# Performance work log

Hardware: AMD Instinct MI355X
Metric: run time of the kernel (lower is better)

## Reference

```python
import jax, jax.numpy as jnp
import numpy as np

LOGISTIC_R = 3.8
COUPLING_ITERS = 5


def _linear_interp(v, L):
    """PyTorch F.interpolate(mode='linear', align_corners=False) along last axis.
    v: [..., K] real -> [..., L] real."""
    K = v.shape[-1]
    pos = (jnp.arange(L, dtype=jnp.float32) + 0.5) * (K / L) - 0.5
    pos = jnp.clip(pos, 0.0, K - 1)  # torch clamps src coords into range
    i0 = jnp.floor(pos).astype(jnp.int32)
    i1 = jnp.minimum(i0 + 1, K - 1)
    w = pos - i0
    return v[..., i0] * (1.0 - w) + v[..., i1] * w


def setup_inputs() -> dict:
    key = jax.random.key(0)
    ks = jax.random.split(key, 4)
    B, Cin, Cout, L, K = 16, 64, 64, 8192, 64
    return {
        "x_real": jax.random.normal(ks[0], (B, Cin, L), jnp.float32),
        "x_imag": jax.random.normal(ks[1], (B, Cin, L), jnp.float32),
        "kernel_real": jax.random.normal(ks[2], (Cout, Cin, K), jnp.float32),
        "kernel_imag": jax.random.normal(ks[3], (Cout, Cin, K), jnp.float32),
        "alpha_D": jnp.ones((1,), jnp.float32),
    }


def reference(x_real, x_imag, kernel_real, kernel_imag, alpha_D):
    x = x_real + 1j * x_imag  # [B, Cin, L] complex64
    L = x.shape[-1]

    # --- logistic self-coupling on magnitude (per-batch min/max over (C, L)) ---
    mag = jnp.abs(x)
    phase = jnp.angle(x)
    mmin = mag.min(axis=(-1, -2), keepdims=True)
    mmax = mag.max(axis=(-1, -2), keepdims=True)
    xn = (mag - mmin) / (mmax - mmin + 1e-10)
    for _ in range(COUPLING_ITERS):
        xn = LOGISTIC_R * xn * (1.0 - xn)
    mag_c = xn * (mmax - mmin) + mmin
    x_coupled = mag_c * jnp.exp(1j * phase)

    # --- spectral conv: FFT, per-pair kernel interpolation, complex MAC ---
    x_fft = jnp.fft.fft(x_coupled, axis=-1)  # [B, Cin, L]
    kfft = jnp.fft.fft(kernel_real + 1j * kernel_imag, axis=-1)  # [O, I, K]
    kmag = _linear_interp(jnp.abs(kfft), L)    # [O, I, L]
    kph = _linear_interp(jnp.angle(kfft), L)   # [O, I, L]
    kint = kmag * jnp.exp(1j * kph)            # [O, I, L] complex64
    out_fft = jnp.einsum('bjl,ijl->bil', x_fft, kint)  # replaces O*I python loop
    out = jnp.fft.ifft(out_fft, axis=-1)  # [B, O, L]

    # --- optical probe activation: sin(omega*0 + phi0 + alpha_D * lambda) ---
    theta = alpha_D[0] * jnp.arange(L, dtype=jnp.float32)
    act = jnp.sin(theta)  # omega*t = 0, phi0 = 0
    return out * act
```

## Files before the change

### kernel.cpp

```cpp
#include <hip/hip_runtime.h>
#include <hip/hip_fp16.h>
#include <hip/hip_bf16.h>
#include <math.h>

#define L 8192
#define LOG2L 13
#define B 16
#define CIN 64
#define COUT 64
#define KK 64

#define PI_F 3.14159265358979323846f

typedef float f4v __attribute__((ext_vector_type(4)));
typedef short s8v __attribute__((ext_vector_type(8)));

__device__ __forceinline__ int PHI(int n) { return n ^ ((((n >> 5) ^ (n >> 9)) & 15) << 1); }

__device__ __forceinline__ void nsincos(float ang, float* sn, float* cs) {
    float r = ang * 0.15915494309189535f;
    r = r - floorf(r);
    *sn = __builtin_amdgcn_sinf(r);
    *cs = __builtin_amdgcn_cosf(r);
}

__device__ __forceinline__ unsigned short f2bf(float f) {
    unsigned u = __builtin_bit_cast(unsigned, f);
    u += 0x7FFFu + ((u >> 16) & 1u);
    return (unsigned short)(u >> 16);
}
__device__ __forceinline__ unsigned pkbf(float a, float b) {
    unsigned ua = __builtin_bit_cast(unsigned, a) + 0x8000u;
    unsigned ub = __builtin_bit_cast(unsigned, b) + 0x8000u;
    return (ub & 0xFFFF0000u) | (ua >> 16);
}
__device__ __forceinline__ float bf_lo(unsigned u) {
    return __builtin_bit_cast(float, u << 16);
}
__device__ __forceinline__ float bf_hi(unsigned u) {
    return __builtin_bit_cast(float, u & 0xFFFF0000u);
}

template<int INV>
__device__ __forceinline__ void bfly4(float& u0r, float& u0i, float& u1r, float& u1i,
                                      float& v0r, float& v0i, float& v1r, float& v1i,
                                      float w1r, float w1i, float w2r, float w2i) {
    float A0r = u0r + v0r, A0i = u0i + v0i;
    float t0r = u0r - v0r, t0i = u0i - v0i;
    float B0r = t0r * w1r - t0i * w1i, B0i = t0r * w1i + t0i * w1r;
    float A1r = u1r + v1r, A1i = u1i + v1i;
    float t1r = u1r - v1r, t1i = u1i - v1i;
    float wr = t1r * w1r - t1i * w1i, wi = t1r * w1i + t1i * w1r;
    float B1r = INV ? -wi : wi;
    float B1i = INV ? wr : -wr;
    u0r = A0r + A1r; u0i = A0i + A1i;
    float d0r = A0r - A1r, d0i = A0i - A1i;
    u1r = d0r * w2r - d0i * w2i; u1i = d0r * w2i + d0i * w2r;
    v0r = B0r + B1r; v0i = B0i + B1i;
    float d1r = B0r - B1r, d1i = B0i - B1i;
    v1r = d1r * w2r - d1i * w2i; v1i = d1r * w2i + d1i * w2r;
}

template<int INV>
__device__ __forceinline__ void radix16(float* xr, float* xi, float wc, float ws) {
    const float C8 = 0.9238795325112867f, S8 = 0.3826834323650898f, C4 = 0.7071067811865476f;
    float e1r = C8, e1i = INV ? S8 : -S8;
    float e2r = C4, e2i = INV ? C4 : -C4;
    float e3r = S8, e3i = INV ? C8 : -C8;
    float a1r[4], a1i[4], a2r[4], a2i[4];
    a1r[0] = wc;                    a1i[0] = ws;
    a1r[1] = wc * e1r - ws * e1i;   a1i[1] = wc * e1i + ws * e1r;
    a1r[2] = wc * e2r - ws * e2i;   a1i[2] = wc * e2i + ws * e2r;
    a1r[3] = wc * e3r - ws * e3i;   a1i[3] = wc * e3i + ws * e3r;
#pragma unroll
    for (int q = 0; q < 4; ++q) {
        a2r[q] = a1r[q] * a1r[q] - a1i[q] * a1i[q];
        a2i[q] = 2.f * a1r[q] * a1i[q];
    }
    float b1r = a2r[0] * a2r[0] - a2i[0] * a2i[0], b1i = 2.f * a2r[0] * a2i[0];
    float b2r = b1r * b1r - b1i * b1i, b2i = 2.f * b1r * b1i;
#pragma unroll
    for (int q = 0; q < 4; ++q)
        bfly4<INV>(xr[q], xi[q], xr[q + 4], xi[q + 4], xr[q + 8], xi[q + 8],
                   xr[q + 12], xi[q + 12], a1r[q], a1i[q], a2r[q], a2i[q]);
#pragma unroll
    for (int c = 0; c < 4; ++c)
        bfly4<INV>(xr[4 * c], xi[4 * c], xr[4 * c + 1], xi[4 * c + 1],
                   xr[4 * c + 2], xi[4 * c + 2], xr[4 * c + 3], xi[4 * c + 3],
                   b1r, b1i, b2r, b2i);
}

__global__ __launch_bounds__(256) void k_reduce1(const float* __restrict__ xr,
                                                 const float* __restrict__ xi,
                                                 float* __restrict__ pmin,
                                                 float* __restrict__ pmax) {
    int bid = blockIdx.x;
    int batch = bid >> 6, slice = bid & 63;
    size_t base = (size_t)batch * CIN * L + (size_t)slice * L;
    int tid = threadIdx.x;
    float mn = 3.4e38f, mx = 0.0f;
    for (int r = 0; r < 32; ++r) {
        int idx = r * 256 + tid;
        float a = xr[base + idx], b = xi[base + idx];
        float m = sqrtf(a * a + b * b);
        mn = fminf(mn, m);
        mx = fmaxf(mx, m);
    }
    __shared__ float smn[4], smx[4];
    for (int off = 32; off >= 1; off >>= 1) {
        mn = fminf(mn, __shfl_down(mn, off));
        mx = fmaxf(mx, __shfl_down(mx, off));
    }
    int wave = tid >> 6;
    if ((tid & 63) == 0) { smn[wave] = mn; smx[wave] = mx; }
    __syncthreads();
    if (tid == 0) {
        for (int w = 1; w < 4; ++w) { mn = fminf(mn, smn[w]); mx = fmaxf(mx, smx[w]); }
        pmin[bid] = mn;
        pmax[bid] = mx;
    }
}

__global__ __launch_bounds__(64) void k_reduce2(const float* __restrict__ pmin,
                                                const float* __restrict__ pmax,
                                                float* __restrict__ mmin,
                                                float* __restrict__ mmax) {
    int b = blockIdx.x, t = threadIdx.x;
    float mn = pmin[b * 64 + t], mx = pmax[b * 64 + t];
    for (int off = 32; off >= 1; off >>= 1) {
        mn = fminf(mn, __shfl_down(mn, off));
        mx = fmaxf(mx, __shfl_down(mx, off));
    }
    if (t == 0) { mmin[b] = mn; mmax[b] = mx; }
}

__global__ __launch_bounds__(64) void k_kstats(const float* __restrict__ kr,
                                               const float* __restrict__ ki,
                                               float* __restrict__ Pmag,
                                               float* __restrict__ Pph) {
    int row = blockIdx.x;
    int k = threadIdx.x;
    __shared__ float sr[64], si[64];
    sr[k] = kr[row * 64 + k];
    si[k] = ki[row * 64 + k];
    __syncthreads();
    float ar = 0.f, ai = 0.f;
    for (int n = 0; n < 64; ++n) {
        int m = (n * k) & 63;
        float ang = -2.0f * PI_F * (float)m * (1.0f / 64.0f);
        float s, c;
        __sincosf(ang, &s, &c);
        ar += sr[n] * c - si[n] * s;
        ai += sr[n] * s + si[n] * c;
    }
    float mag = sqrtf(ar * ar + ai * ai);
    float ph = atan2f(ai, ar);
    int io = row >> 6, jn = row & 63;
    int ic = io >> 4, l15 = io & 15;
    int jc = jn >> 5, hi = (jn >> 3) & 3, e = jn & 7;
    int lane = hi * 16 + l15;
    size_t off = (size_t)k * 4096 + (ic * 2 + jc) * 512 + lane * 8 + e;
    Pmag[off] = mag;
    Pph[off] = ph;
    if (k == 63) {
        Pmag[off + 4096] = mag;
        Pph[off + 4096] = ph;
    }
}

__global__ __launch_bounds__(512) void k_fwd(const float* __restrict__ xr,
                                             const float* __restrict__ xi,
                                             const float* __restrict__ mmin_,
                                             const float* __restrict__ mmax_,
                                             unsigned* __restrict__ Xd) {
    __shared__ unsigned sPk[L];
    int row = blockIdx.x;
    int b = row >> 6;
    int tid = threadIdx.x;
    float mmin = mmin_[b], mmax = mmax_[b];
    float span = mmax - mmin;
    float invden = 1.0f / (span + 1e-10f);
    size_t base = (size_t)row * L;

    float vr[16], vi[16];
#pragma unroll
    for (int r = 0; r < 16; ++r) {
        int idx = r * 512 + tid;
        float a = xr[base + idx], c = xi[base + idx];
        float m2 = a * a + c * c;
        float rinv = (m2 > 0.0f) ? __builtin_amdgcn_rsqf(m2) : 0.0f;
        float m = m2 * rinv;
        float xn = (m - mmin) * invden;
#pragma unroll
        for (int it = 0; it < 5; ++it) xn = 3.8f * xn * (1.0f - xn);
        float mc = xn * span + mmin;
        float scale = mc * rinv;
        vr[r] = a * scale;
        vi[r] = c * scale;
    }
    {
        const float ER = 0.9238795325112867f, EI = -0.3826834323650898f;
        float wr_, wi_;
        nsincos(-PI_F * (float)tid * (1.0f / 4096.0f), &wi_, &wr_);
#pragma unroll
        for (int r = 0; r < 8; ++r) {
            float ar = vr[r], ai = vi[r], br = vr[r + 8], bi = vi[r + 8];
            vr[r] = ar + br; vi[r] = ai + bi;
            float dr = ar - br, di = ai - bi;
            vr[r + 8] = dr * wr_ - di * wi_;
            vi[r + 8] = dr * wi_ + di * wr_;
            float nr = wr_ * ER - wi_ * EI;
            wi_ = wr_ * EI + wi_ * ER;
            wr_ = nr;
        }
    }
#pragma unroll
    for (int r = 0; r < 16; ++r)
        sPk[PHI(r * 512 + tid)] = pkbf(vr[r], vi[r]);
    __syncthreads();

    {
        int j1 = tid & 255, bA = (tid >> 8) << 12;
#pragma unroll
        for (int m = 0; m < 16; ++m) {
            unsigned u = sPk[PHI(bA + j1 + (m << 8))];
            vr[m] = bf_lo(u); vi[m] = bf_hi(u);
        }
        float sn, cs;
        nsincos(-PI_F * (float)j1 * (1.0f / 2048.0f), &sn, &cs);
        radix16<0>(vr, vi, cs, sn);
#pragma unroll
        for (int m = 0; m < 16; ++m)
            sPk[PHI(bA + j1 + (m << 8))] = pkbf(vr[m], vi[m]);
    }
    __syncthreads();
    {
        int j1 = tid & 15, bB = (tid >> 4) << 8;
#pragma unroll
        for (int m = 0; m < 16; ++m) {
            unsigned u = sPk[PHI(bB + j1 + (m << 4))];
            vr[m] = bf_lo(u); vi[m] = bf_hi(u);
        }
        float sn, cs;
        nsincos(-PI_F * (float)j1 * (1.0f / 128.0f), &sn, &cs);
        radix16<0>(vr, vi, cs, sn);
#pragma unroll
        for (int m = 0; m < 16; ++m)
            sPk[PHI(bB + j1 + (m << 4))] = pkbf(vr[m], vi[m]);
    }
    __syncthreads();
    {
        uint2* s2 = (uint2*)sPk;
#pragma unroll
        for (int m = 0; m < 8; ++m) {
            int a = PHI(tid * 16 + 2 * m) >> 1;
            uint2 u2 = s2[a];
            vr[2 * m] = bf_lo(u2.x); vi[2 * m] = bf_hi(u2.x);
            vr[2 * m + 1] = bf_lo(u2.y); vi[2 * m + 1] = bf_hi(u2.y);
        }
        radix16<0>(vr, vi, 1.0f, 0.0f);
#pragma unroll
        for (int m = 0; m < 8; ++m) {
            int a = PHI(tid * 16 + 2 * m) >> 1;
            s2[a] = make_uint2(pkbf(vr[2 * m], vi[2 * m]),
                               pkbf(vr[2 * m + 1], vi[2 * m + 1]));
        }
    }
    __syncthreads();

    {
        int rt = (int)(__brev((unsigned)tid) >> 23);
        unsigned o16[16];
#pragma unroll
        for (int r = 0; r < 16; ++r) {
            int pi = (int)(__brev((unsigned)r) >> 28);
            o16[pi] = sPk[PHI(r * 512 + rt)];
        }
        size_t ob = (size_t)tid * 16384 + (size_t)row * 16;
#pragma unroll
        for (int k = 0; k < 4; ++k)
            *(uint4*)&Xd[ob + 4 * k] = make_uint4(o16[4 * k], o16[4 * k + 1],
                                                  o16[4 * k + 2], o16[4 * k + 3]);
    }
}

#define PBG 8
#define REG 4624
__global__ __launch_bounds__(256) void k_gemm(const unsigned* __restrict__ X,
                                              const float* __restrict__ Pmag,
                                              const float* __restrict__ Pph,
                                              unsigned* __restrict__ outd) {
    __shared__ uint4 ldsbuf[(PBG * REG) / 16];
    char* lds = (char*)ldsbuf;
    int tid = threadIdx.x;
    int bid = blockIdx.x;
    int pwin = ((bid & 7) << 7) + (bid >> 3);
    int p0 = pwin * PBG;
    int half = pwin & 1;
    const unsigned* src = X + (size_t)(pwin >> 1) * 16384 + half * 8;

#pragma unroll
    for (int k = 0; k < 8; ++k) {
        int u = k * 256 + tid;
        int row = u >> 1;
        int g = u & 1;
        uint4 v = *(const uint4*)&src[(size_t)row * 16 + g * 4];
        int base = (row >> 6) * 144 + (row & 63) * 2;
        unsigned dw[4] = {v.x, v.y, v.z, v.w};
#pragma unroll
        for (int c = 0; c < 4; ++c) {
            int pl = g * 4 + c;
            *(unsigned short*)&lds[pl * REG + base] = (unsigned short)(dw[c] & 0xFFFFu);
            *(unsigned short*)&lds[pl * REG + 2304 + base] = (unsigned short)(dw[c] >> 16);
        }
    }
    __syncthreads();

    int lane = tid & 63, wid = tid >> 6;
    int l15 = lane & 15, l4 = lane >> 4;

    int pA = p0 + wid * 2;
    float posA = ((float)pA + 0.5f) * (1.0f / 128.0f) - 0.5f;
    posA = fmaxf(posA, 0.0f);
    int i0k = (int)posA;
    bool clampv = (i0k >= KK - 1);
    float wq[2];
#pragma unroll
    for (int q = 0; q < 2; ++q) {
        float pos = ((float)(pA + q) + 0.5f) * (1.0f / 128.0f) - 0.5f;
        pos = fmaxf(pos, 0.0f);
        wq[q] = clampv ? 0.0f : (pos - (float)i0k);
    }
    const float* mb0 = Pmag + (size_t)i0k * 4096;
    const float* pb0 = Pph + (size_t)i0k * 4096;

    f4v accR[2][4], accI[2][4];
#pragma unroll
    for (int q = 0; q < 2; ++q)
#pragma unroll
        for (int ic = 0; ic < 4; ++ic) { accR[q][ic] = (f4v)0.0f; accI[q][ic] = (f4v)0.0f; }

#pragma unroll
    for (int jc = 0; jc < 2; ++jc) {
        int jb2 = (jc * 32 + l4 * 8) * 2;
        s8v xR0 = *(const s8v*)&lds[(wid * 2 + 0) * REG + l15 * 144 + jb2];
        s8v xI0 = *(const s8v*)&lds[(wid * 2 + 0) * REG + 2304 + l15 * 144 + jb2];
        s8v xR1 = *(const s8v*)&lds[(wid * 2 + 1) * REG + l15 * 144 + jb2];
        s8v xI1 = *(const s8v*)&lds[(wid * 2 + 1) * REG + 2304 + l15 * 144 + jb2];
#pragma unroll
        for (int ic = 0; ic < 4; ++ic) {
            int tb = (ic * 2 + jc) * 512 + lane * 8;
            float4 m0a = *(const float4*)(mb0 + tb);
            float4 m0b = *(const float4*)(mb0 + tb + 4);
            float4 m1a = *(const float4*)(mb0 + 4096 + tb);
            float4 m1b = *(const float4*)(mb0 + 4096 + tb + 4);
            float4 q0a = *(const float4*)(pb0 + tb);
            float4 q0b = *(const float4*)(pb0 + tb + 4);
            float4 q1a = *(const float4*)(pb0 + 4096 + tb);
            float4 q1b = *(const float4*)(pb0 + 4096 + tb + 4);
            float m0v[8] = {m0a.x, m0a.y, m0a.z, m0a.w, m0b.x, m0b.y, m0b.z, m0b.w};
            float m1v[8] = {m1a.x, m1a.y, m1a.z, m1a.w, m1b.x, m1b.y, m1b.z, m1b.w};
            float q0v[8] = {q0a.x, q0a.y, q0a.z, q0a.w, q0b.x, q0b.y, q0b.z, q0b.w};
            float q1v[8] = {q1a.x, q1a.y, q1a.z, q1a.w, q1b.x, q1b.y, q1b.z, q1b.w};
#pragma unroll
            for (int q = 0; q < 2; ++q) {
                float w = wq[q];
                float kr[8], ki[8];
#pragma unroll
                for (int e = 0; e < 8; ++e) {
                    float mm = m0v[e] + (m1v[e] - m0v[e]) * w;
                    float ph = q0v[e] + (q1v[e] - q0v[e]) * w;
                    float sn, cs;
                    nsincos(ph, &sn, &cs);
                    kr[e] = mm * cs;
                    ki[e] = mm * sn;
                }
                union { unsigned u[4]; s8v v; } kR, kIp, kIn;
#pragma unroll
                for (int t = 0; t < 4; ++t) {
                    kR.u[t] = pkbf(kr[2 * t], kr[2 * t + 1]);
                    kIp.u[t] = pkbf(ki[2 * t], ki[2 * t + 1]);
                    kIn.u[t] = kIp.u[t] ^ 0x80008000u;
                }
                s8v xR = q ? xR1 : xR0;
                s8v xI = q ? xI1 : xI0;
                accR[q][ic] = __builtin_amdgcn_mfma_f32_16x16x32_bf16(xR, kR.v, accR[q][ic], 0, 0, 0);
                accR[q][ic] = __builtin_amdgcn_mfma_f32_16x16x32_bf16(xI, kIn.v, accR[q][ic], 0, 0, 0);
                accI[q][ic] = __builtin_amdgcn_mfma_f32_16x16x32_bf16(xR, kIp.v, accI[q][ic], 0, 0, 0);
                accI[q][ic] = __builtin_amdgcn_mfma_f32_16x16x32_bf16(xI, kR.v, accI[q][ic], 0, 0, 0);
            }
        }
    }

#pragma unroll
    for (int q = 0; q < 2; ++q) {
        int pp = wid * 2 + q;
#pragma unroll
        for (int ic = 0; ic < 4; ++ic)
#pragma unroll
            for (int e = 0; e < 4; ++e) {
                int ro = (l4 * 4 + e) * 64 + ic * 16 + l15;
                unsigned val = ((unsigned)f2bf(accI[q][ic][e]) << 16) | f2bf(accR[q][ic][e]);
                *(unsigned*)&lds[pp * REG + ro * 4] = val;
            }
    }
    __syncthreads();

#pragma unroll
    for (int k = 0; k < 32; ++k) {
        int row = k * 32 + (tid >> 3);
        unsigned v = *(const unsigned*)&lds[(tid & 7) * REG + row * 4];
        outd[(size_t)row * 8192 + p0 + (tid & 7)] = v;
    }
}

__global__ __launch_bounds__(512) void k_ifft(const __hip_bfloat162* __restrict__ outfft,
                                              const float* __restrict__ alpha_,
                                              float* __restrict__ out) {
    __shared__ float sRe[L];
    __shared__ float sIm[L];
    int row = blockIdx.x;
    int tid = threadIdx.x;
    float alpha = alpha_[0];
    size_t base = (size_t)row * L;

    float vr[16], vi[16];
#pragma unroll
    for (int r = 0; r < 16; ++r) {
        __hip_bfloat162 v = outfft[base + r * 512 + tid];
        vr[r] = __bfloat162float(v.x);
        vi[r] = __bfloat162float(v.y);
    }
    {
        const float ER = 0.9238795325112867f, EI = 0.3826834323650898f;
        float wr_, wi_;
        nsincos(PI_F * (float)tid * (1.0f / 4096.0f), &wi_, &wr_);
#pragma unroll
        for (int r = 0; r < 8; ++r) {
            float ar = vr[r], ai = vi[r], br = vr[r + 8], bi = vi[r + 8];
            vr[r] = ar + br; vi[r] = ai + bi;
            float dr = ar - br, di = ai - bi;
            vr[r + 8] = dr * wr_ - di * wi_;
            vi[r + 8] = dr * wi_ + di * wr_;
            float nr = wr_ * ER - wi_ * EI;
            wi_ = wr_ * EI + wi_ * ER;
            wr_ = nr;
        }
    }
#pragma unroll
    for (int r = 0; r < 16; ++r) {
        int a = PHI(r * 512 + tid);
        sRe[a] = vr[r]; sIm[a] = vi[r];
    }
    __syncthreads();

    {
        int j1 = tid & 255, bA = (tid >> 8) << 12;
#pragma unroll
        for (int m = 0; m < 16; ++m) {
            int a = PHI(bA + j1 + (m << 8));
            vr[m] = sRe[a]; vi[m] = sIm[a];
        }
        float sn, cs;
        nsincos(PI_F * (float)j1 * (1.0f / 2048.0f), &sn, &cs);
        radix16<1>(vr, vi, cs, sn);
#pragma unroll
        for (int m = 0; m < 16; ++m) {
            int a = PHI(bA + j1 + (m << 8));
            sRe[a] = vr[m]; sIm[a] = vi[m];
        }
    }
    __syncthreads();
    {
        int j1 = tid & 15, bB = (tid >> 4) << 8;
#pragma unroll
        for (int m = 0; m < 16; ++m) {
            int a = PHI(bB + j1 + (m << 4));
            vr[m] = sRe[a]; vi[m] = sIm[a];
        }
        float sn, cs;
        nsincos(PI_F * (float)j1 * (1.0f / 128.0f), &sn, &cs);
        radix16<1>(vr, vi, cs, sn);
#pragma unroll
        for (int m = 0; m < 16; ++m) {
            int a = PHI(bB + j1 + (m << 4));
            sRe[a] = vr[m]; sIm[a] = vi[m];
        }
    }
    __syncthreads();
    {
        float2* f2R = (float2*)sRe;
        float2* f2I = (float2*)sIm;
#pragma unroll
        for (int m = 0; m < 8; ++m) {
            int a = PHI(tid * 16 + 2 * m) >> 1;
            float2 vR = f2R[a], vI = f2I[a];
            vr[2 * m] = vR.x; vr[2 * m + 1] = vR.y;
            vi[2 * m] = vI.x; vi[2 * m + 1] = vI.y;
        }
        radix16<1>(vr, vi, 1.0f, 0.0f);
#pragma unroll
        for (int m = 0; m < 8; ++m) {
            int a = PHI(tid * 16 + 2 * m) >> 1;
            f2R[a] = make_float2(vr[2 * m], vr[2 * m + 1]);
            f2I[a] = make_float2(vi[2 * m], vi[2 * m + 1]);
        }
    }
    __syncthreads();

    {
        int rt = (int)(__brev((unsigned)tid) >> 23);
        const float invN = 1.0f / (float)L;
        float t16[16];
#pragma unroll
        for (int r = 0; r < 16; ++r) {
            int a = PHI(r * 512 + rt);
            int pi = (int)(__brev((unsigned)r) >> 28);
            t16[pi] = sRe[a];
        }
        float sA, cA, s1, c1;
        nsincos(alpha * (float)(tid * 16), &sA, &cA);
        nsincos(alpha, &s1, &c1);
        float o[16];
#pragma unroll
        for (int pi = 0; pi < 16; ++pi) {
            o[pi] = t16[pi] * sA * invN;
            float ns = sA * c1 + cA * s1;
            cA = cA * c1 - sA * s1;
            sA = ns;
        }
        float* dst = out + base + (size_t)tid * 16;
#pragma unroll
        for (int k = 0; k < 4; ++k)
            *(float4*)&dst[4 * k] = make_float4(o[4 * k], o[4 * k + 1],
                                                o[4 * k + 2], o[4 * k + 3]);
    }
}

extern "C" void kernel_launch(void* const* d_in, const int* in_sizes, int n_in,
                              void* d_out, int out_size, void* d_ws, size_t ws_size,
                              hipStream_t stream) {
    const float* xr = (const float*)d_in[0];
    const float* xi = (const float*)d_in[1];
    const float* kr = (const float*)d_in[2];
    const float* ki = (const float*)d_in[3];
    const float* alpha = (const float*)d_in[4];
    float* out = (float*)d_out;

    char* ws = (char*)d_ws;
    size_t OFFT_BYTES = (size_t)B * COUT * L * 4;
    size_t TBL_BYTES = (size_t)65 * 4096 * 4;
    unsigned* outfft_d = (unsigned*)ws;
    float* Pmag = (float*)(ws + OFFT_BYTES);
    float* Pph  = (float*)(ws + OFFT_BYTES + TBL_BYTES);
    float* pmin = (float*)(ws + OFFT_BYTES + 2 * TBL_BYTES);
    float* pmax = pmin + 1024;
    float* mmin = pmax + 1024;
    float* mmax = mmin + 16;

    unsigned* Xd = (unsigned*)d_out;

    hipLaunchKernelGGL(k_reduce1, dim3(1024), dim3(256), 0, stream, xr, xi, pmin, pmax);
    hipLaunchKernelGGL(k_reduce2, dim3(16), dim3(64), 0, stream, pmin, pmax, mmin, mmax);
    hipLaunchKernelGGL(k_kstats, dim3(4096), dim3(64), 0, stream, kr, ki, Pmag, Pph);
    hipLaunchKernelGGL(k_fwd, dim3(1024), dim3(512), 0, stream, xr, xi, mmin, mmax, Xd);
    hipLaunchKernelGGL(k_gemm, dim3(1024), dim3(256), 0, stream, Xd, Pmag, Pph, outfft_d);
    hipLaunchKernelGGL(k_ifft, dim3(1024), dim3(512), 0, stream,
                       (const __hip_bfloat162*)outfft_d, alpha, out);
}
```

Baseline: 119.9 us.

## Split spectral GEMM across 8 waves with one frequency each, pack LDS writes

k_gemm now launches 512 threads, and each wave handles a single frequency bin instead of two. This halves per-wave accumulator and register pressure and doubles the waves per block, aiming for better latency hiding of the sin/cos kernel synthesis and the MFMAs. The LDS staging loop now merges two adjacent rows into one 32-bit write instead of separate 16-bit stores, cutting the number of LDS store instructions. In exchange, the interpolation tables are loaded by twice as many waves, since the two frequencies that used to share one table load are now split. The interpolation clamp is also evaluated per frequency rather than per pair.

New measurement: 123.6 us. +3.1%, slower.

```diff
diff --git a/kernel.cpp b/kernel.cpp
--- a/kernel.cpp
+++ b/kernel.cpp
@@ -286,7 +286,7 @@
 
 #define PBG 8
 #define REG 4624
-__global__ __launch_bounds__(256) void k_gemm(const unsigned* __restrict__ X,
+__global__ __launch_bounds__(512) void k_gemm(const unsigned* __restrict__ X,
                                               const float* __restrict__ Pmag,
                                               const float* __restrict__ Pph,
                                               unsigned* __restrict__ outd) {
@@ -300,53 +300,48 @@
     const unsigned* src = X + (size_t)(pwin >> 1) * 16384 + half * 8;
 
 #pragma unroll
-    for (int k = 0; k < 8; ++k) {
-        int u = k * 256 + tid;
-        int row = u >> 1;
-        int g = u & 1;
-        uint4 v = *(const uint4*)&src[(size_t)row * 16 + g * 4];
-        int base = (row >> 6) * 144 + (row & 63) * 2;
-        unsigned dw[4] = {v.x, v.y, v.z, v.w};
+    for (int k = 0; k < 2; ++k) {
+        int i2 = k * 512 + tid;
+        int rp = i2 >> 1;
+        int g = i2 & 1;
+        uint4 vA = *(const uint4*)&src[(size_t)(2 * rp) * 16 + g * 4];
+        uint4 vB = *(const uint4*)&src[(size_t)(2 * rp + 1) * 16 + g * 4];
+        int base = ((2 * rp) >> 6) * 144 + ((2 * rp) & 63) * 2;
+        unsigned a4[4] = {vA.x, vA.y, vA.z, vA.w};
+        unsigned b4[4] = {vB.x, vB.y, vB.z, vB.w};
 #pragma unroll
         for (int c = 0; c < 4; ++c) {
             int pl = g * 4 + c;
-            *(unsigned short*)&lds[pl * REG + base] = (unsigned short)(dw[c] & 0xFFFFu);
-            *(unsigned short*)&lds[pl * REG + 2304 + base] = (unsigned short)(dw[c] >> 16);
+            unsigned re = (a4[c] & 0xFFFFu) | (b4[c] << 16);
+            unsigned im = (a4[c] >> 16) | (b4[c] & 0xFFFF0000u);
+            *(unsigned*)&lds[pl * REG + base] = re;
+            *(unsigned*)&lds[pl * REG + 2304 + base] = im;
         }
     }
     __syncthreads();
 
     int lane = tid & 63, wid = tid >> 6;
     int l15 = lane & 15, l4 = lane >> 4;
-
-    int pA = p0 + wid * 2;
-    float posA = ((float)pA + 0.5f) * (1.0f / 128.0f) - 0.5f;
-    posA = fmaxf(posA, 0.0f);
-    int i0k = (int)posA;
-    bool clampv = (i0k >= KK - 1);
-    float wq[2];
-#pragma unroll
-    for (int q = 0; q < 2; ++q) {
-        float pos = ((float)(pA + q) + 0.5f) * (1.0f / 128.0f) - 0.5f;
-        pos = fmaxf(pos, 0.0f);
-        wq[q] = clampv ? 0.0f : (pos - (float)i0k);
-    }
+    int pp = wid;
+    int p = p0 + pp;
+
+    float pos = ((float)p + 0.5f) * (1.0f / 128.0f) - 0.5f;
+    pos = fmaxf(pos, 0.0f);
+    int i0k = (int)pos;
+    float w = pos - (float)i0k;
+    if (i0k >= KK - 1) { i0k = KK - 1; w = 0.0f; }
     const float* mb0 = Pmag + (size_t)i0k * 4096;
     const float* pb0 = Pph + (size_t)i0k * 4096;
 
-    f4v accR[2][4], accI[2][4];
-#pragma unroll
-    for (int q = 0; q < 2; ++q)
-#pragma unroll
-        for (int ic = 0; ic < 4; ++ic) { accR[q][ic] = (f4v)0.0f; accI[q][ic] = (f4v)0.0f; }
+    f4v accR[4], accI[4];
+#pragma unroll
+    for (int ic = 0; ic < 4; ++ic) { accR[ic] = (f4v)0.0f; accI[ic] = (f4v)0.0f; }
 
 #pragma unroll
     for (int jc = 0; jc < 2; ++jc) {
         int jb2 = (jc * 32 + l4 * 8) * 2;
-        s8v xR0 = *(const s8v*)&lds[(wid * 2 + 0) * REG + l15 * 144 + jb2];
-        s8v xI0 = *(const s8v*)&lds[(wid * 2 + 0) * REG + 2304 + l15 * 144 + jb2];
-        s8v xR1 = *(const s8v*)&lds[(wid * 2 + 1) * REG + l15 * 144 + jb2];
-        s8v xI1 = *(const s8v*)&lds[(wid * 2 + 1) * REG + 2304 + l15 * 144 + jb2];
+        s8v xR = *(const s8v*)&lds[pp * REG + l15 * 144 + jb2];
+        s8v xI = *(const s8v*)&lds[pp * REG + 2304 + l15 * 144 + jb2];
 #pragma unroll
         for (int ic = 0; ic < 4; ++ic) {
             int tb = (ic * 2 + jc) * 512 + lane * 8;
@@ -362,53 +357,43 @@
             float m1v[8] = {m1a.x, m1a.y, m1a.z, m1a.w, m1b.x, m1b.y, m1b.z, m1b.w};
             float q0v[8] = {q0a.x, q0a.y, q0a.z, q0a.w, q0b.x, q0b.y, q0b.z, q0b.w};
             float q1v[8] = {q1a.x, q1a.y, q1a.z, q1a.w, q1b.x, q1b.y, q1b.z, q1b.w};
-#pragma unroll
-            for (int q = 0; q < 2; ++q) {
-                float w = wq[q];
-                float kr[8], ki[8];
-#pragma unroll
-                for (int e = 0; e < 8; ++e) {
-                    float mm = m0v[e] + (m1v[e] - m0v[e]) * w;
-                    float ph = q0v[e] + (q1v[e] - q0v[e]) * w;
-                    float sn, cs;
-                    nsincos(ph, &sn, &cs);
-                    kr[e] = mm * cs;
-                    ki[e] = mm * sn;
-                }
-                union { unsigned u[4]; s8v v; } kR, kIp, kIn;
-#pragma unroll
-                for (int t = 0; t < 4; ++t) {
-                    kR.u[t] = pkbf(kr[2 * t], kr[2 * t + 1]);
-                    kIp.u[t] = pkbf(ki[2 * t], ki[2 * t + 1]);
-                    kIn.u[t] = kIp.u[t] ^ 0x80008000u;
-                }
-                s8v xR = q ? xR1 : xR0;
-                s8v xI = q ? xI1 : xI0;
-                accR[q][ic] = __builtin_amdgcn_mfma_f32_16x16x32_bf16(xR, kR.v, accR[q][ic], 0, 0, 0);
-                accR[q][ic] = __builtin_amdgcn_mfma_f32_16x16x32_bf16(xI, kIn.v, accR[q][ic], 0, 0, 0);
-                accI[q][ic] = __builtin_amdgcn_mfma_f32_16x16x32_bf16(xR, kIp.v, accI[q][ic], 0, 0, 0);
-                accI[q][ic] = __builtin_amdgcn_mfma_f32_16x16x32_bf16(xI, kR.v, accI[q][ic], 0, 0, 0);
+            float kr[8], ki[8];
+#pragma unroll
+            for (int e = 0; e < 8; ++e) {
+                float mm = m0v[e] + (m1v[e] - m0v[e]) * w;
+                float ph = q0v[e] + (q1v[e] - q0v[e]) * w;
+                float sn, cs;
+                nsincos(ph, &sn, &cs);
+                kr[e] = mm * cs;
+                ki[e] = mm * sn;
             }
-        }
-    }
-
-#pragma unroll
-    for (int q = 0; q < 2; ++q) {
-        int pp = wid * 2 + q;
-#pragma unroll
-        for (int ic = 0; ic < 4; ++ic)
-#pragma unroll
-            for (int e = 0; e < 4; ++e) {
-                int ro = (l4 * 4 + e) * 64 + ic * 16 + l15;
-                unsigned val = ((unsigned)f2bf(accI[q][ic][e]) << 16) | f2bf(accR[q][ic][e]);
-                *(unsigned*)&lds[pp * REG + ro * 4] = val;
+            union { unsigned u[4]; s8v v; } kR, kIp, kIn;
+#pragma unroll
+            for (int t = 0; t < 4; ++t) {
+                kR.u[t] = pkbf(kr[2 * t], kr[2 * t + 1]);
+                kIp.u[t] = pkbf(ki[2 * t], ki[2 * t + 1]);
+                kIn.u[t] = kIp.u[t] ^ 0x80008000u;
             }
-    }
-    __syncthreads();
-
-#pragma unroll
-    for (int k = 0; k < 32; ++k) {
-        int row = k * 32 + (tid >> 3);
+            accR[ic] = __builtin_amdgcn_mfma_f32_16x16x32_bf16(xR, kR.v, accR[ic], 0, 0, 0);
+            accR[ic] = __builtin_amdgcn_mfma_f32_16x16x32_bf16(xI, kIn.v, accR[ic], 0, 0, 0);
+            accI[ic] = __builtin_amdgcn_mfma_f32_16x16x32_bf16(xR, kIp.v, accI[ic], 0, 0, 0);
+            accI[ic] = __builtin_amdgcn_mfma_f32_16x16x32_bf16(xI, kR.v, accI[ic], 0, 0, 0);
+        }
+    }
+
+#pragma unroll
+    for (int ic = 0; ic < 4; ++ic)
+#pragma unroll
+        for (int e = 0; e < 4; ++e) {
+            int ro = (l4 * 4 + e) * 64 + ic * 16 + l15;
+            unsigned val = ((unsigned)f2bf(accI[ic][e]) << 16) | f2bf(accR[ic][e]);
+            *(unsigned*)&lds[pp * REG + ro * 4] = val;
+        }
+    __syncthreads();
+
+#pragma unroll
+    for (int k = 0; k < 16; ++k) {
+        int row = k * 64 + (tid >> 3);
         unsigned v = *(const unsigned*)&lds[(tid & 7) * REG + row * 4];
         outd[(size_t)row * 8192 + p0 + (tid & 7)] = v;
     }
@@ -564,7 +549,7 @@
     hipLaunchKernelGGL(k_reduce2, dim3(16), dim3(64), 0, stream, pmin, pmax, mmin, mmax);
     hipLaunchKernelGGL(k_kstats, dim3(4096), dim3(64), 0, stream, kr, ki, Pmag, Pph);
     hipLaunchKernelGGL(k_fwd, dim3(1024), dim3(512), 0, stream, xr, xi, mmin, mmax, Xd);
-    hipLaunchKernelGGL(k_gemm, dim3(1024), dim3(256), 0, stream, Xd, Pmag, Pph, outfft_d);
+    hipLaunchKernelGGL(k_gemm, dim3(1024), dim3(512), 0, stream, Xd, Pmag, Pph, outfft_d);
     hipLaunchKernelGGL(k_ifft, dim3(1024), dim3(512), 0, stream,
                        (const __hip_bfloat162*)outfft_d, alpha, out);
 }
```
